# Kernel optimization log

Hardware: AMD Instinct MI355X
Metric: run time of the kernel (lower is better)

## Reference

```python
import math
import jax, jax.numpy as jnp
import numpy as np

NC, NA, NL = 80, 3, 3
NO = NC + 5
STRIDES = (8, 16, 32)
BS, IN_CH, IMG, NT = 8, 256, 640, 200
BALANCE = (4.0, 1.0, 0.25)
G, ANCHOR_T, EPS = 0.5, 2.91, 1e-9
LBOX_W, LOBJ_W, LCLS_W, POS_BAL = 0.05, 1.0, 0.5, 0.5
OFF = np.array([[0., 0.], [1., 0.], [0., 1.], [-1., 0.], [0., -1.]], np.float32) * G
_h = np.sqrt(np.array([0.5, 1.0, 2.0], np.float32))  # h_ratios = sqrt(aspect_ratios)
# per layer anchors: (w, h) = (size/h_ratio, size*h_ratio), divided by stride (grid units)
ANCHORS = np.stack([np.stack([s / _h, s * _h], 1) / st
                    for s, st in zip((32., 64., 128.), STRIDES)]).astype(np.float32)  # [NL,NA,2]


def setup_inputs():
    key = jax.random.key(0)
    ks = jax.random.split(key, 16)
    inp = {}
    for i, st in enumerate(STRIDES):
        n = IMG // st
        inp[f"feat{i}"] = jax.random.normal(ks[i], (BS, IN_CH, n, n), jnp.float32)
        inp[f"w{i}"] = jax.random.normal(ks[3 + i], (NO * NA, IN_CH), jnp.float32) * 0.02
        b = np.zeros((NA, NO), np.float32)
        b[:, 4] += math.log(8 / (640 / st) ** 2)          # _initialize_biases obj prior
        b[:, 5:] += math.log(0.6 / (NC - 0.99))           # _initialize_biases cls prior
        inp[f"b{i}"] = jnp.asarray(b.reshape(-1))
    # targets: [NT, 6] = (image_idx, class, cx, cy, w, h) normalized to [0,1]
    img = jax.random.randint(ks[6], (NT, 1), 0, BS).astype(jnp.float32)
    cls = jax.random.randint(ks[7], (NT, 1), 0, NC).astype(jnp.float32)
    xy = jax.random.uniform(ks[8], (NT, 2), minval=0.05, maxval=0.95)
    wh = jax.random.uniform(ks[9], (NT, 2), minval=0.02, maxval=0.3)
    inp["targets"] = jnp.concatenate([img, cls, xy, wh], 1)
    return inp


def _head(x, w, b):
    # 1x1 conv == channel GEMM, then view/permute to [bs, na, ny, nx, no]
    y = jnp.einsum('bchw,oc->bohw', x, w) + b[None, :, None, None]
    bs, _, ny, nx = y.shape
    return y.reshape(bs, NA, NO, ny, nx).transpose(0, 1, 3, 4, 2)


def _ciou(b1, b2):
    # b1, b2: [n,4] in center-xywh format; YOLOv5-style CIoU
    x1, y1, w1, h1 = b1[:, 0], b1[:, 1], b1[:, 2], b1[:, 3]
    x2, y2, w2, h2 = b2[:, 0], b2[:, 1], b2[:, 2], b2[:, 3]
    b1x1, b1x2, b1y1, b1y2 = x1 - w1 / 2, x1 + w1 / 2, y1 - h1 / 2, y1 + h1 / 2
    b2x1, b2x2, b2y1, b2y2 = x2 - w2 / 2, x2 + w2 / 2, y2 - h2 / 2, y2 + h2 / 2
    inter = (jnp.maximum(jnp.minimum(b1x2, b2x2) - jnp.maximum(b1x1, b2x1), 0.0)
             * jnp.maximum(jnp.minimum(b1y2, b2y2) - jnp.maximum(b1y1, b2y1), 0.0))
    union = w1 * h1 + w2 * h2 - inter + EPS
    iou = inter / union
    cw = jnp.maximum(b1x2, b2x2) - jnp.minimum(b1x1, b2x1)  # enclosing box
    ch = jnp.maximum(b1y2, b2y2) - jnp.minimum(b1y1, b2y1)
    c2 = cw ** 2 + ch ** 2 + EPS
    rho2 = ((b2x1 + b2x2 - b1x1 - b1x2) ** 2 + (b2y1 + b2y2 - b1y1 - b1y2) ** 2) / 4
    v = (4.0 / math.pi ** 2) * (jnp.arctan(w2 / (h2 + EPS)) - jnp.arctan(w1 / (h1 + EPS))) ** 2
    alpha = jax.lax.stop_gradient(v / (v - iou + (1.0 + EPS)))
    return iou - (rho2 / c2 + v * alpha)


def _bce_pw(logits, t, pw):
    # BCEWithLogits with pos_weight: pw*t*(-logsigmoid(x)) + (1-t)*softplus(x)
    return pw * t * jax.nn.softplus(-logits) + (1.0 - t) * jax.nn.softplus(logits)


def _forward(feats, ws, bias, targets):
    anchors = jnp.asarray(ANCHORS)
    off = jnp.asarray(OFF)
    ai = jnp.arange(NA, dtype=jnp.float32)
    # targets replicated per anchor with anchor index appended: [NA, NT, 7]
    tg = jnp.concatenate([jnp.broadcast_to(targets[None], (NA, NT, 6)),
                          jnp.broadcast_to(ai[:, None, None], (NA, NT, 1))], 2)
    lbox = jnp.float32(0.0); lobj = jnp.float32(0.0); lcls = jnp.float32(0.0)
    for i in range(NL):
        pi = _head(feats[i], ws[i], bias[i])  # [BS, NA, ny, nx, NO]
        ny, nx = pi.shape[2], pi.shape[3]
        gain = jnp.array([1, 1, nx, ny, nx, ny, 1], jnp.float32)
        t = tg * gain  # grid units, [NA, NT, 7]
        # anchor-ratio filter (torch: t = t[j]) expressed as a validity mask
        r = t[..., 4:6] / anchors[i][:, None, :]
        m_anchor = (jnp.max(jnp.maximum(r, 1.0 / r), -1) < ANCHOR_T).reshape(-1)  # [NA*NT]
        tf = t.reshape(-1, 7)
        gxy = tf[:, 2:4]
        gxi = jnp.array([nx, ny], jnp.float32) - gxy
        near = (gxy % 1.0 < G) & (gxy > 1.0)
        far = (gxi % 1.0 < G) & (gxi > 1.0)
        sel = jnp.stack([jnp.ones_like(near[:, 0]), near[:, 0], near[:, 1], far[:, 0], far[:, 1]])
        mask = (sel & m_anchor[None]).reshape(-1)  # [5*NA*NT] valid candidates
        N = tf.shape[0]
        t5 = jnp.broadcast_to(tf[None], (5, N, 7)).reshape(-1, 7)
        offs = jnp.broadcast_to(off[:, None, :], (5, N, 2)).reshape(-1, 2)
        b_idx = t5[:, 0].astype(jnp.int32)
        c_idx = t5[:, 1].astype(jnp.int32)
        a_idx = t5[:, 6].astype(jnp.int32)
        gxy5, gwh5 = t5[:, 2:4], t5[:, 4:6]
        gij = (gxy5 - offs).astype(jnp.int32)  # trunc, values are positive -> matches .long()
        gi = jnp.clip(gij[:, 0], 0, nx - 1)
        gj = jnp.clip(gij[:, 1], 0, ny - 1)
        tbox = jnp.concatenate([gxy5 - gij.astype(jnp.float32), gwh5], 1)
        anch = anchors[i][a_idx]
        # gather predictions at sparse (b, a, gj, gi)
        ps = pi[b_idx, a_idx, gj, gi]  # [M, NO]
        pxy = jax.nn.sigmoid(ps[:, :2]) * 2.0 - 0.5
        pwh = (jax.nn.sigmoid(ps[:, 2:4]) * 2.0) ** 2 * anch
        iou = _ciou(jnp.concatenate([pxy, pwh], 1), tbox)
        fmask = mask.astype(jnp.float32)
        n_valid = fmask.sum()
        lbox = lbox + jnp.sum(fmask * (1.0 - iou)) / jnp.maximum(n_valid, 1.0)
        # scatter tobj; invalid rows routed to padded batch slot BS then sliced off
        b_s = jnp.where(mask, b_idx, BS)
        tobj = jnp.zeros((BS + 1, NA, ny, nx), jnp.float32)
        tobj = tobj.at[b_s, a_idx, gj, gi].set(
            jax.lax.stop_gradient(jnp.maximum(iou, 0.0)))[:BS]
        # classification BCE with dynamically computed pos_weight
        tcl = jax.nn.one_hot(c_idx, NC, dtype=jnp.float32)
        pw_c = (n_valid * (NC - 1)) * POS_BAL / jnp.maximum(n_valid, 2.0)
        bce_c = _bce_pw(ps[:, 5:], tcl, pw_c)
        lcls = lcls + jnp.sum(fmask[:, None] * bce_c) / jnp.maximum(n_valid * NC, 1.0)
        # objectness BCE over the full map with dynamic pos_weight
        fg_o = (tobj > 0).sum().astype(jnp.float32)
        bg_o = (tobj == 0).sum().astype(jnp.float32)
        pw_o = bg_o * POS_BAL / jnp.maximum(fg_o, 2.0)
        lobj = lobj + jnp.mean(_bce_pw(pi[..., 4], tobj, pw_o)) * BALANCE[i]
    return jnp.stack([lbox * LBOX_W, lobj * LOBJ_W, lcls * LCLS_W])


def reference(feat0, feat1, feat2, w0, w1, w2, b0, b1, b2, targets):
    return _forward((feat0, feat1, feat2), (w0, w1, w2), (b0, b1, b2), targets)
```

## Files before the change

### kernel.cpp

```cpp
#include <hip/hip_runtime.h>
#include <stdint.h>

#define NCLS 80
#define NO 85
#define CIN 256
#define ANCHOR_T 2.91f
#define EPSF 1e-9f

#define S0 153600
#define S1_ 38400
#define S2_ 9600
#define LB0 0
#define LB1 153600
#define LB2 192000

#define NGATHB 375
#define NHEADB 1050
#define NB (NGATHB + NHEADB)
#define NREC (NGATHB * 24)

#define WS_TOBJ_OFF 0
#define WS_HSP_OFF  806400
#define WS_GP_OFF   810608
#define WS_REC_OFF  816608

__device__ __constant__ float AW_[3] = {5.656854249f, 4.0f, 2.828427125f};
__device__ __constant__ float AH_[3] = {2.828427125f, 4.0f, 5.656854249f};

__device__ __forceinline__ float softplusf(float x) {
    return fmaxf(x, 0.0f) + log1pf(expf(-fabsf(x)));
}
__device__ __forceinline__ float sigmoidf_(float x) {
    return 1.0f / (1.0f + expf(-x));
}
__device__ __forceinline__ float wave_red(float v) {
    #pragma unroll
    for (int o = 32; o > 0; o >>= 1) v += __shfl_down(v, o);
    return v;
}
__device__ __forceinline__ void async_load16(const void* g, void* l) {
    __builtin_amdgcn_global_load_lds(
        (const __attribute__((address_space(1))) void*)g,
        (__attribute__((address_space(3))) void*)l, 16, 0, 0);
}

struct HeadSm {
    float  lw[3][CIN];
    float4 stage[64 * 16];
    float  part[16][16][13];
    float  ws_[4];
};
struct GathSm {
    float lf[8][260];
    float pb[8][3][5];
    float tbx[8][4];
    int   vm[8], eb[8], egi[8], egj[8], ec[8];
    int   kblk;
    float r1[24], r2[24];
    float wsum[2][4];
};
union AllSm { HeadSm h; GathSm g; };

template<int PERQ, int BLK0>
__device__ __forceinline__ void head_impl(
    const float* __restrict__ f, const float* __restrict__ w, const float* __restrict__ bi,
    float* __restrict__ hsp, int hb, int tid, HeadSm& sm)
{
    for (int i = tid; i < 3 * CIN; i += 256) {
        int a = i >> 8, c = i & 255;
        sm.lw[a][c] = w[(a * NO + 4) * CIN + c];
    }

    const int wv4 = tid >> 6;
    const int ln  = tid & 63;
    const int q0  = (hb - BLK0) * 16;
    const int qlane = q0 + (ln & 15);
    const int blane = qlane / PERQ;
    const int rlane = qlane - blane * PERQ;
    const float4* f4 = (const float4*)f;

    const int qt = tid & 15;
    const int cg = tid >> 4;

    float a0[12];
    #pragma unroll
    for (int j = 0; j < 12; ++j) a0[j] = 0.f;

    for (int g = 0; g < 4; ++g) {
        #pragma unroll
        for (int i = 0; i < 4; ++i) {
            int cl = wv4 * 16 + i * 4 + (ln >> 4);
            int c  = g * 64 + cl;
            const float4* gp4 = f4 + ((blane * CIN + c) * PERQ + rlane);
            float4* ldst = &sm.stage[(wv4 * 16 + i * 4) * 16];
            async_load16(gp4, ldst);
        }
        __syncthreads();
        #pragma unroll
        for (int j = 0; j < 4; ++j) {
            float4 fv = sm.stage[(cg * 4 + j) * 16 + qt];
            int c = g * 64 + cg * 4 + j;
            #pragma unroll
            for (int a = 0; a < 3; ++a) {
                float wvv = sm.lw[a][c];
                a0[a*4+0] += fv.x * wvv;
                a0[a*4+1] += fv.y * wvv;
                a0[a*4+2] += fv.z * wvv;
                a0[a*4+3] += fv.w * wvv;
            }
        }
        __syncthreads();
    }

    #pragma unroll
    for (int v = 0; v < 12; ++v) sm.part[cg][qt][v] = a0[v];
    __syncthreads();

    float sp = 0.f;
    if (tid < 192) {
        int q2 = tid / 12, v = tid - q2 * 12;
        float s = 0.f;
        #pragma unroll
        for (int c2 = 0; c2 < 16; ++c2) s += sm.part[c2][q2][v];
        s += bi[(v >> 2) * NO + 4];
        sp = softplusf(s);
    }
    sp = wave_red(sp);
    if ((tid & 63) == 0) sm.ws_[tid >> 6] = sp;
    __syncthreads();
    if (tid == 0)
        hsp[hb] = sm.ws_[0] + sm.ws_[1] + sm.ws_[2] + sm.ws_[3];
}

__device__ void gath_impl(
    const float* __restrict__ f, const float* __restrict__ w, const float* __restrict__ bi,
    const float* __restrict__ targets,
    unsigned* __restrict__ tobj4, float4* __restrict__ gp, int4* __restrict__ recs,
    int bid, int tid, int l, int o, int tile, GathSm& sm)
{
    const int nx = (l == 0) ? 80 : (l == 1) ? 40 : 20;
    const int ny = nx;
    const int plane = nx * ny;
    const int ltb = (l == 0) ? LB0 : (l == 1) ? LB1 : LB2;

    if (tid < 8) {
        const int t = tid;
        const int n = tile * 8 + t;
        const float* tg = targets + n * 6;
        float tb = tg[0], tcl = tg[1];
        float gx = tg[2] * (float)nx, gy = tg[3] * (float)ny;
        float gw = tg[4] * (float)nx, gh = tg[5] * (float)ny;
        float ox = 0.f, oy = 0.f;
        bool s = true;
        if (o == 1)      { s = (fmodf(gx, 1.f) < 0.5f) && (gx > 1.f); ox = 0.5f; }
        else if (o == 2) { s = (fmodf(gy, 1.f) < 0.5f) && (gy > 1.f); oy = 0.5f; }
        else if (o == 3) { float gxi = (float)nx - gx; s = (fmodf(gxi, 1.f) < 0.5f) && (gxi > 1.f); ox = -0.5f; }
        else if (o == 4) { float gyi = (float)ny - gy; s = (fmodf(gyi, 1.f) < 0.5f) && (gyi > 1.f); oy = -0.5f; }
        int vmask = 0;
        if (s) {
            #pragma unroll
            for (int a = 0; a < 3; ++a) {
                float rw = gw / AW_[a], rh = gh / AH_[a];
                float mr = fmaxf(fmaxf(rw, 1.f / rw), fmaxf(rh, 1.f / rh));
                if (mr < ANCHOR_T) vmask |= (1 << a);
            }
        }
        sm.vm[t] = vmask;
        int gi = (int)(gx - ox);
        int gj = (int)(gy - oy);
        sm.tbx[t][0] = gx - (float)gi;
        sm.tbx[t][1] = gy - (float)gj;
        sm.tbx[t][2] = gw;
        sm.tbx[t][3] = gh;
        sm.egi[t] = min(max(gi, 0), nx - 1);
        sm.egj[t] = min(max(gj, 0), ny - 1);
        sm.eb[t]  = (int)tb;
        sm.ec[t]  = (int)tcl;
    }
    __syncthreads();

    if (tid == 0) {
        int k = 0;
        #pragma unroll
        for (int t = 0; t < 8; ++t) k |= sm.vm[t];
        sm.kblk = k;
    }
    __syncthreads();

    if (sm.kblk == 0) {
        if (tid == 0) gp[bid] = make_float4(0.f, 0.f, 0.f, 0.f);
        return;
    }

    {
        const int t  = tid >> 5;
        const int ln = tid & 31;
        if (sm.vm[t]) {
            const float* fb = f + sm.eb[t] * CIN * plane + sm.egj[t] * nx + sm.egi[t];
            #pragma unroll
            for (int k2 = 0; k2 < 8; ++k2) {
                int c = ln + k2 * 32;
                sm.lf[t][c] = fb[c * plane];
            }
        }
    }
    __syncthreads();

    float s1 = 0.f, s2 = 0.f;
    if (tid < 255) {
        const int a  = tid / 85;
        const int oc = tid - a * 85;
        const float bv = bi[tid];
        float dacc[8];
        #pragma unroll
        for (int t = 0; t < 8; ++t) dacc[t] = bv;
        const float4* wr4 = (const float4*)w + tid * 64;
        #pragma unroll 4
        for (int c4 = 0; c4 < 64; ++c4) {
            float4 wv = wr4[c4];
            #pragma unroll
            for (int t = 0; t < 8; ++t) {
                float4 fv = *((const float4*)&sm.lf[t][c4 * 4]);
                dacc[t] += wv.x * fv.x + wv.y * fv.y + wv.z * fv.z + wv.w * fv.w;
            }
        }
        if (oc >= 5) {
            const int cls = oc - 5;
            #pragma unroll
            for (int t = 0; t < 8; ++t) {
                if ((sm.vm[t] >> a) & 1) {
                    if (cls == sm.ec[t]) s1 += softplusf(-dacc[t]);
                    else                 s2 += softplusf(dacc[t]);
                }
            }
        } else {
            #pragma unroll
            for (int t = 0; t < 8; ++t) sm.pb[t][a][oc] = dacc[t];
        }
    }
    s1 = wave_red(s1);
    s2 = wave_red(s2);
    if ((tid & 63) == 0) { sm.wsum[0][tid >> 6] = s1; sm.wsum[1][tid >> 6] = s2; }
    __syncthreads();

    if (tid < 24) {
        const int t = tid & 7;
        const int a = tid >> 3;
        if ((sm.vm[t] >> a) & 1) {
            float px = sigmoidf_(sm.pb[t][a][0]) * 2.f - 0.5f;
            float py = sigmoidf_(sm.pb[t][a][1]) * 2.f - 0.5f;
            float swp = sigmoidf_(sm.pb[t][a][2]) * 2.f; float pw = swp * swp * AW_[a];
            float shp = sigmoidf_(sm.pb[t][a][3]) * 2.f; float ph = shp * shp * AH_[a];
            float tx = sm.tbx[t][0], ty = sm.tbx[t][1], tw = sm.tbx[t][2], th = sm.tbx[t][3];
            float b1x1 = px - pw * 0.5f, b1x2 = px + pw * 0.5f;
            float b1y1 = py - ph * 0.5f, b1y2 = py + ph * 0.5f;
            float b2x1 = tx - tw * 0.5f, b2x2 = tx + tw * 0.5f;
            float b2y1 = ty - th * 0.5f, b2y2 = ty + th * 0.5f;
            float iw = fmaxf(fminf(b1x2, b2x2) - fmaxf(b1x1, b2x1), 0.f);
            float ih = fmaxf(fminf(b1y2, b2y2) - fmaxf(b1y1, b2y1), 0.f);
            float inter = iw * ih;
            float uni = pw * ph + tw * th - inter + EPSF;
            float iou = inter / uni;
            float cw = fmaxf(b1x2, b2x2) - fminf(b1x1, b2x1);
            float chh = fmaxf(b1y2, b2y2) - fminf(b1y1, b2y1);
            float c2 = cw * cw + chh * chh + EPSF;
            float dx = b2x1 + b2x2 - b1x1 - b1x2;
            float dy = b2y1 + b2y2 - b1y1 - b1y2;
            float rho2 = (dx * dx + dy * dy) * 0.25f;
            float dat = atanf(tw / (th + EPSF)) - atanf(pw / (ph + EPSF));
            float v = 0.4052847346f * dat * dat;
            float alpha = v / (v - iou + (1.f + EPSF));
            float ciou = iou - (rho2 / c2 + v * alpha);
            float tt = fmaxf(ciou, 0.f);
            int idx = ltb + ((sm.eb[t] * 3 + a) * ny + sm.egj[t]) * nx + sm.egi[t];
            int n = tile * 8 + t;
            int ek = o * 600 + a * 200 + n;
            int slot = bid * 24 + tid;
            int4 rc; rc.x = idx; rc.y = __float_as_int(sm.pb[t][a][4]); rc.z = __float_as_int(tt); rc.w = 1;
            recs[slot] = rc;
            unsigned pk = 0xC0000000u | ((unsigned)(ek + 1) << 14) | (unsigned)slot;
            atomicMax(&tobj4[idx], pk);
            sm.r1[tid] = 1.f - ciou;
            sm.r2[tid] = 1.f;
        } else {
            sm.r1[tid] = 0.f;
            sm.r2[tid] = 0.f;
        }
    }
    __syncthreads();
    if (tid == 0) {
        float lb = 0.f, nv = 0.f;
        #pragma unroll
        for (int e = 0; e < 24; ++e) { lb += sm.r1[e]; nv += sm.r2[e]; }
        float4 gpv;
        gpv.x = lb; gpv.y = nv;
        gpv.z = sm.wsum[0][0] + sm.wsum[0][1] + sm.wsum[0][2] + sm.wsum[0][3];
        gpv.w = sm.wsum[1][0] + sm.wsum[1][1] + sm.wsum[1][2] + sm.wsum[1][3];
        gp[bid] = gpv;
    }
}

__global__ __launch_bounds__(256) void yolo_main(
    const float* __restrict__ f0, const float* __restrict__ w0, const float* __restrict__ b0,
    const float* __restrict__ f1, const float* __restrict__ w1, const float* __restrict__ b1,
    const float* __restrict__ f2, const float* __restrict__ w2, const float* __restrict__ b2,
    const float* __restrict__ targets,
    unsigned* __restrict__ tobj4, float* __restrict__ hsp,
    float4* __restrict__ gp, int4* __restrict__ recs)
{
    __shared__ AllSm sm;
    const int bid = blockIdx.x;
    const int tid = threadIdx.x;

    if (bid < NGATHB) {
        const int l    = bid / 125;
        const int rem  = bid - l * 125;
        const int o    = rem / 25;
        const int tile = rem - o * 25;
        const float* f  = (l == 0) ? f0 : (l == 1) ? f1 : f2;
        const float* w  = (l == 0) ? w0 : (l == 1) ? w1 : w2;
        const float* bi = (l == 0) ? b0 : (l == 1) ? b1 : b2;
        gath_impl(f, w, bi, targets, tobj4, gp, recs, bid, tid, l, o, tile, sm.g);
    } else {
        const int hb = bid - NGATHB;
        if (hb < 800)       head_impl<1600, 0>  (f0, w0, b0, hsp, hb, tid, sm.h);
        else if (hb < 1000) head_impl<400, 800> (f1, w1, b1, hsp, hb, tid, sm.h);
        else                head_impl<100, 1000>(f2, w2, b2, hsp, hb, tid, sm.h);
    }
}

__global__ __launch_bounds__(1024) void yolo_fin(
    unsigned* __restrict__ tobj4,
    const float* __restrict__ hsp, const float4* __restrict__ gp,
    const int4* __restrict__ recs, float* __restrict__ out)
{
    const int tid = threadIdx.x;
    __shared__ float red[24];
    if (tid < 24) red[tid] = 0.f;
    __syncthreads();

    float t2b[3] = {0,0,0};
    for (int i = tid; i < NHEADB; i += 1024) {
        int l = (i < 800) ? 0 : (i < 1000) ? 1 : 2;
        t2b[l] += hsp[i];
    }
    float lb[3] = {0,0,0}, nv[3] = {0,0,0}, c1[3] = {0,0,0}, c2[3] = {0,0,0};
    for (int i = tid; i < NGATHB; i += 1024) {
        int l = i / 125;
        float4 g = gp[i];
        lb[l] += g.x; nv[l] += g.y; c1[l] += g.z; c2[l] += g.w;
    }
    float T1[3] = {0,0,0}, T2s[3] = {0,0,0}, fgc[3] = {0,0,0};
    for (int i = tid; i < NREC; i += 1024) {
        int4 r = recs[i];
        if (r.w != 1) continue;
        unsigned old = atomicExch(&tobj4[r.x], 0u);
        if (old >= 0xC0000000u) {
            int ws_ = (int)(old & 0x3FFFu);
            float tw = __int_as_float(recs[ws_].z);
            float x  = __int_as_float(r.y);
            int l = (r.x >= LB2) ? 2 : (r.x >= LB1) ? 1 : 0;
            T1[l]  += tw * softplusf(-x);
            T2s[l] += tw * softplusf(x);
            fgc[l] += (tw > 0.f) ? 1.f : 0.f;
        }
    }
    #pragma unroll
    for (int l = 0; l < 3; ++l) {
        if (lb[l]  != 0.f) atomicAdd(&red[l*8+0], lb[l]);
        if (nv[l]  != 0.f) atomicAdd(&red[l*8+1], nv[l]);
        if (c1[l]  != 0.f) atomicAdd(&red[l*8+2], c1[l]);
        if (c2[l]  != 0.f) atomicAdd(&red[l*8+3], c2[l]);
        if (t2b[l] != 0.f) atomicAdd(&red[l*8+4], t2b[l]);
        if (T1[l]  != 0.f) atomicAdd(&red[l*8+5], T1[l]);
        if (T2s[l] != 0.f) atomicAdd(&red[l*8+6], T2s[l]);
        if (fgc[l] != 0.f) atomicAdd(&red[l*8+7], fgc[l]);
    }
    __syncthreads();
    if (tid == 0) {
        const float bal[3]   = {4.f, 1.f, 0.25f};
        const float numel[3] = {(float)S0, (float)S1_, (float)S2_};
        float lbox = 0.f, lobj = 0.f, lcls = 0.f;
        for (int i = 0; i < 3; ++i) {
            float lbs = red[i*8+0];
            float nvv = red[i*8+1];
            float s1  = red[i*8+2];
            float s2  = red[i*8+3];
            float T2b = red[i*8+4];
            float T1v = red[i*8+5];
            float T2  = T2b - red[i*8+6];
            float fg  = red[i*8+7];
            lbox += lbs / fmaxf(nvv, 1.f);
            float pwc = nvv * (float)(NCLS - 1) * 0.5f / fmaxf(nvv, 2.f);
            lcls += (pwc * s1 + s2) / fmaxf(nvv * (float)NCLS, 1.f);
            float bg = numel[i] - fg;
            float pwo = bg * 0.5f / fmaxf(fg, 2.f);
            lobj += (pwo * T1v + T2) / numel[i] * bal[i];
        }
        out[0] = lbox * 0.05f;
        out[1] = lobj * 1.0f;
        out[2] = lcls * 0.5f;
    }
}

extern "C" void kernel_launch(void* const* d_in, const int* in_sizes, int n_in,
                              void* d_out, int out_size, void* d_ws, size_t ws_size,
                              hipStream_t stream) {
    (void)in_sizes; (void)n_in; (void)out_size; (void)ws_size;
    const float* f0 = (const float*)d_in[0];
    const float* w0 = (const float*)d_in[1];
    const float* b0 = (const float*)d_in[2];
    const float* f1 = (const float*)d_in[3];
    const float* w1 = (const float*)d_in[4];
    const float* b1 = (const float*)d_in[5];
    const float* f2 = (const float*)d_in[6];
    const float* w2 = (const float*)d_in[7];
    const float* b2 = (const float*)d_in[8];
    const float* tg = (const float*)d_in[9];
    float* out = (float*)d_out;

    char* ws = (char*)d_ws;
    unsigned* tobj4 = (unsigned*)(ws + WS_TOBJ_OFF);
    float* hsp      = (float*)(ws + WS_HSP_OFF);
    float4* gp      = (float4*)(ws + WS_GP_OFF);
    int4* recs      = (int4*)(ws + WS_REC_OFF);

    yolo_main<<<dim3(NB), dim3(256), 0, stream>>>(f0, w0, b0, f1, w1, b1, f2, w2, b2, tg,
                                                  tobj4, hsp, gp, recs);
    yolo_fin<<<dim3(1), dim3(1024), 0, stream>>>(tobj4, hsp, gp, recs, out);
}
```

Measured before the change: 174.2 us.

## Double-buffer head feature loads per wave and split final reduction across blocks

The objectness head now gives each wave its own double-buffered LDS stage, with explicit waitcnt fences in place of block-wide syncthreads, so global loads for the next channel chunk overlap the FMAs on the current one. Partial sums are reduced with cross-lane shuffles instead of an LDS partial array. The single-block finalize kernel is split into a 96-block first pass that writes per-block partials and a one-block second pass, so the record and atomic-exchange loop runs in parallel. This adds one kernel launch and relies on hand-coded waitcnt encodings being correct.

```diff
diff --git a/kernel.cpp b/kernel.cpp
--- a/kernel.cpp
+++ b/kernel.cpp
@@ -18,11 +18,13 @@
 #define NHEADB 1050
 #define NB (NGATHB + NHEADB)
 #define NREC (NGATHB * 24)
+#define NFIN1 96
 
 #define WS_TOBJ_OFF 0
 #define WS_HSP_OFF  806400
 #define WS_GP_OFF   810608
 #define WS_REC_OFF  816608
+#define WS_PART_OFF 960608
 
 __device__ __constant__ float AW_[3] = {5.656854249f, 4.0f, 2.828427125f};
 __device__ __constant__ float AH_[3] = {2.828427125f, 4.0f, 5.656854249f};
@@ -44,10 +46,13 @@
         (__attribute__((address_space(3))) void*)l, 16, 0, 0);
 }
 
+#define WAIT_VM2   0x0F72
+#define WAIT_VM0   0x0F70
+#define WAIT_LGKM0 0xC07F
+
 struct HeadSm {
     float  lw[3][CIN];
-    float4 stage[64 * 16];
-    float  part[16][16][13];
+    float4 stage[4 * 256];
     float  ws_[4];
 };
 struct GathSm {
@@ -70,63 +75,74 @@
         int a = i >> 8, c = i & 255;
         sm.lw[a][c] = w[(a * NO + 4) * CIN + c];
     }
+    __syncthreads();
 
     const int wv4 = tid >> 6;
     const int ln  = tid & 63;
-    const int q0  = (hb - BLK0) * 16;
-    const int qlane = q0 + (ln & 15);
-    const int blane = qlane / PERQ;
-    const int rlane = qlane - blane * PERQ;
-    const float4* f4 = (const float4*)f;
-
-    const int qt = tid & 15;
-    const int cg = tid >> 4;
-
-    float a0[12];
+    const int q   = ln & 3;
+    const int cl  = ln >> 2;
+    const int qL  = (hb - BLK0) * 16 + wv4 * 4 + q;
+    const int bb  = qL / PERQ;
+    const int rr  = qL - bb * PERQ;
+    const float4* f4  = (const float4*)f;
+    const float4* f4l = f4 + (bb * CIN + cl) * PERQ + rr;
+    float4* stW = sm.stage + wv4 * 256;
+
+    float acc[12];
     #pragma unroll
-    for (int j = 0; j < 12; ++j) a0[j] = 0.f;
-
-    for (int g = 0; g < 4; ++g) {
+    for (int j = 0; j < 12; ++j) acc[j] = 0.f;
+
+    auto ISSUE = [&](int r) {
+        float4* dst = stW + (r & 1) * 128;
+        const float4* g0 = f4l + (r * 32) * PERQ;
+        async_load16(g0, dst);
+        async_load16(g0 + 16 * PERQ, dst + 64);
+    };
+
+    ISSUE(0);
+    ISSUE(1);
+    #pragma unroll
+    for (int r = 0; r < 8; ++r) {
+        if (r < 7) __builtin_amdgcn_s_waitcnt(WAIT_VM2);
+        else       __builtin_amdgcn_s_waitcnt(WAIT_VM0);
+        __builtin_amdgcn_sched_barrier(0);
+        const float4* bp = stW + (r & 1) * 128;
+        float4 v0 = bp[ln];
+        float4 v1 = bp[64 + ln];
+        const int c = r * 32 + cl;
         #pragma unroll
-        for (int i = 0; i < 4; ++i) {
-            int cl = wv4 * 16 + i * 4 + (ln >> 4);
-            int c  = g * 64 + cl;
-            const float4* gp4 = f4 + ((blane * CIN + c) * PERQ + rlane);
-            float4* ldst = &sm.stage[(wv4 * 16 + i * 4) * 16];
-            async_load16(gp4, ldst);
-        }
-        __syncthreads();
-        #pragma unroll
-        for (int j = 0; j < 4; ++j) {
-            float4 fv = sm.stage[(cg * 4 + j) * 16 + qt];
-            int c = g * 64 + cg * 4 + j;
-            #pragma unroll
-            for (int a = 0; a < 3; ++a) {
-                float wvv = sm.lw[a][c];
-                a0[a*4+0] += fv.x * wvv;
-                a0[a*4+1] += fv.y * wvv;
-                a0[a*4+2] += fv.z * wvv;
-                a0[a*4+3] += fv.w * wvv;
-            }
-        }
-        __syncthreads();
+        for (int a = 0; a < 3; ++a) {
+            float wa = sm.lw[a][c];
+            float wb = sm.lw[a][c + 16];
+            acc[a*4+0] += v0.x * wa + v1.x * wb;
+            acc[a*4+1] += v0.y * wa + v1.y * wb;
+            acc[a*4+2] += v0.z * wa + v1.z * wb;
+            acc[a*4+3] += v0.w * wa + v1.w * wb;
+        }
+        if (r + 2 < 8) {
+            __builtin_amdgcn_s_waitcnt(WAIT_LGKM0);
+            __builtin_amdgcn_sched_barrier(0);
+            ISSUE(r + 2);
+        }
     }
 
     #pragma unroll
-    for (int v = 0; v < 12; ++v) sm.part[cg][qt][v] = a0[v];
-    __syncthreads();
-
+    for (int j = 0; j < 12; ++j) {
+        float v = acc[j];
+        v += __shfl_xor(v, 4);
+        v += __shfl_xor(v, 8);
+        v += __shfl_xor(v, 16);
+        v += __shfl_xor(v, 32);
+        acc[j] = v;
+    }
     float sp = 0.f;
-    if (tid < 192) {
-        int q2 = tid / 12, v = tid - q2 * 12;
-        float s = 0.f;
-        #pragma unroll
-        for (int c2 = 0; c2 < 16; ++c2) s += sm.part[c2][q2][v];
-        s += bi[(v >> 2) * NO + 4];
+    if (ln < 48) {
+        int j = ln >> 2;
+        float s = acc[j] + bi[(j >> 2) * NO + 4];
         sp = softplusf(s);
     }
     sp = wave_red(sp);
-    if ((tid & 63) == 0) sm.ws_[tid >> 6] = sp;
+    if (ln == 0) sm.ws_[wv4] = sp;
     __syncthreads();
     if (tid == 0)
         hsp[hb] = sm.ws_[0] + sm.ws_[1] + sm.ws_[2] + sm.ws_[3];
@@ -329,35 +345,35 @@
     }
 }
 
-__global__ __launch_bounds__(1024) void yolo_fin(
-    unsigned* __restrict__ tobj4,
-    const float* __restrict__ hsp, const float4* __restrict__ gp,
-    const int4* __restrict__ recs, float* __restrict__ out)
+__global__ __launch_bounds__(256) void yolo_fin1(
+    unsigned* __restrict__ tobj4, const float* __restrict__ hsp,
+    const float4* __restrict__ gp, const int4* __restrict__ recs,
+    float* __restrict__ part)
 {
-    const int tid = threadIdx.x;
+    const int bid = blockIdx.x, tid = threadIdx.x;
     __shared__ float red[24];
     if (tid < 24) red[tid] = 0.f;
     __syncthreads();
 
     float t2b[3] = {0,0,0};
-    for (int i = tid; i < NHEADB; i += 1024) {
+    for (int i = bid * 256 + tid; i < NHEADB; i += NFIN1 * 256) {
         int l = (i < 800) ? 0 : (i < 1000) ? 1 : 2;
         t2b[l] += hsp[i];
     }
     float lb[3] = {0,0,0}, nv[3] = {0,0,0}, c1[3] = {0,0,0}, c2[3] = {0,0,0};
-    for (int i = tid; i < NGATHB; i += 1024) {
+    for (int i = bid * 256 + tid; i < NGATHB; i += NFIN1 * 256) {
         int l = i / 125;
         float4 g = gp[i];
         lb[l] += g.x; nv[l] += g.y; c1[l] += g.z; c2[l] += g.w;
     }
     float T1[3] = {0,0,0}, T2s[3] = {0,0,0}, fgc[3] = {0,0,0};
-    for (int i = tid; i < NREC; i += 1024) {
+    for (int i = bid * 256 + tid; i < NREC; i += NFIN1 * 256) {
         int4 r = recs[i];
         if (r.w != 1) continue;
         unsigned old = atomicExch(&tobj4[r.x], 0u);
         if (old >= 0xC0000000u) {
-            int ws_ = (int)(old & 0x3FFFu);
-            float tw = __int_as_float(recs[ws_].z);
+            int wsl = (int)(old & 0x3FFFu);
+            float tw = __int_as_float(recs[wsl].z);
             float x  = __int_as_float(r.y);
             int l = (r.x >= LB2) ? 2 : (r.x >= LB1) ? 1 : 0;
             T1[l]  += tw * softplusf(-x);
@@ -375,6 +391,23 @@
         if (T1[l]  != 0.f) atomicAdd(&red[l*8+5], T1[l]);
         if (T2s[l] != 0.f) atomicAdd(&red[l*8+6], T2s[l]);
         if (fgc[l] != 0.f) atomicAdd(&red[l*8+7], fgc[l]);
+    }
+    __syncthreads();
+    if (tid < 24) part[bid * 24 + tid] = red[tid];
+}
+
+__global__ __launch_bounds__(256) void yolo_fin2(
+    const float* __restrict__ part, float* __restrict__ out)
+{
+    const int tid = threadIdx.x;
+    __shared__ float red[24];
+    if (tid < 24) red[tid] = 0.f;
+    __syncthreads();
+    if (tid < 240) {
+        int j = tid % 24;
+        float s = 0.f;
+        for (int b = tid / 24; b < NFIN1; b += 10) s += part[b * 24 + j];
+        atomicAdd(&red[j], s);
     }
     __syncthreads();
     if (tid == 0) {
@@ -424,8 +457,10 @@
     float* hsp      = (float*)(ws + WS_HSP_OFF);
     float4* gp      = (float4*)(ws + WS_GP_OFF);
     int4* recs      = (int4*)(ws + WS_REC_OFF);
+    float* part     = (float*)(ws + WS_PART_OFF);
 
     yolo_main<<<dim3(NB), dim3(256), 0, stream>>>(f0, w0, b0, f1, w1, b1, f2, w2, b2, tg,
                                                   tobj4, hsp, gp, recs);
-    yolo_fin<<<dim3(1), dim3(1024), 0, stream>>>(tobj4, hsp, gp, recs, out);
-}
+    yolo_fin1<<<dim3(NFIN1), dim3(256), 0, stream>>>(tobj4, hsp, gp, recs, part);
+    yolo_fin2<<<dim3(1), dim3(256), 0, stream>>>(part, out);
+}
```

Result: faster. 154.7 us (-11.2%).
